# Kernel optimization log

Measured on AMD Instinct MI355X. Metric: run time of the kernel, lower is better.

Reference implementation:

```python
import jax, jax.numpy as jnp
import numpy as np

# Dims: B samples, D=2048 backbone feature dim (resnet50 fc.in_features),
B, D, G, R, K, C = 16384, 2048, 8, 6, 3, 16


def setup_inputs() -> dict:
    key = jax.random.key(0)
    k0, k1, k2, k3 = jax.random.split(key, 4)
    feats = jax.random.normal(k0, (B, D), dtype=jnp.float32)          # backbone output (dropout=eval identity)
    roi_ids = jax.random.randint(k1, (B,), 0, G)                       # per-sample routing id (roi_names)
    W_reg = jax.random.normal(k2, (G, R, D), dtype=jnp.float32) * 0.02  # reg_heads[roi].weight
    b_reg = jnp.zeros((G, R), dtype=jnp.float32)                       # reg_heads[roi].bias
    W_cls = jax.random.normal(k3, (G, K, C, D), dtype=jnp.float32) * 0.02  # cls_heads[roi][k].weight
    b_cls = jnp.zeros((G, K, C), dtype=jnp.float32)                    # cls_heads[roi][k].bias
    return {"feats": feats, "roi_ids": roi_ids, "W_reg": W_reg, "b_reg": b_reg,
            "W_cls": W_cls, "b_cls": b_cls}


def reference(feats, roi_ids, W_reg, b_reg, W_cls, b_cls):
    # Original loop applies, per sample i, the Linear heads of roi_names[i].
    # Vectorized: compute all-ROI head outputs densely, then gather the routed one.
    # (Same math per sample; dropout is identity in eval mode.)
    reg_all = jnp.einsum('bd,grd->bgr', feats, W_reg) + b_reg[None]        # [B, G, R]
    cls_all = jnp.einsum('bd,gkcd->bgkc', feats, W_cls) + b_cls[None]      # [B, G, K, C]
    reg = jnp.take_along_axis(reg_all, roi_ids[:, None, None], axis=1)[:, 0]            # [B, R]
    cls = jnp.take_along_axis(cls_all, roi_ids[:, None, None, None], axis=1)[:, 0]      # [B, K, C]
    return reg, cls
```

## Files before the change

### kernel.cpp

```cpp
#include <hip/hip_runtime.h>
#include <hip/hip_bf16.h>

#define NB   16384
#define ND   2048
#define NG   8
#define NR   6
#define NKC  48
#define NOUT 54
#define KW   512
#define NT16 (NB / 16 + NG)
#define LROW 136
#define BM   32
#define KC   128
#define NCH  (ND / KC)
#define MAXT (NB / BM + NG)

typedef __attribute__((ext_vector_type(8))) short short8_t;
typedef __attribute__((ext_vector_type(4))) float f32x4;

__device__ __forceinline__ unsigned short f2bf(float x) {
    union { float f; unsigned u; } v; v.f = x;
    unsigned r = v.u + 0x7FFFu + ((v.u >> 16) & 1u);
    return (unsigned short)(r >> 16);
}

__device__ __forceinline__ short8_t cvt8(float4 a, float4 b) {
    short8_t s;
    s[0] = (short)f2bf(a.x); s[1] = (short)f2bf(a.y);
    s[2] = (short)f2bf(a.z); s[3] = (short)f2bf(a.w);
    s[4] = (short)f2bf(b.x); s[5] = (short)f2bf(b.y);
    s[6] = (short)f2bf(b.z); s[7] = (short)f2bf(b.w);
    return s;
}

__device__ __forceinline__ short8_t as_s8(float4 v) {
    union { float4 f; short8_t s; } u; u.f = v; return u.s;
}

#define WAITV(N) do { asm volatile("s_waitcnt vmcnt(" #N ")" ::: "memory"); \
                      __builtin_amdgcn_sched_barrier(0); } while (0)

__global__ void hist_kernel(const int* __restrict__ roi, int* __restrict__ counts) {
    int i = blockIdx.x * 256 + threadIdx.x;
    int g = roi[i];
    int lane = threadIdx.x & 63;
    #pragma unroll
    for (int gg = 0; gg < NG; ++gg) {
        unsigned long long m = __ballot(g == gg);
        if (m && lane == (int)(__ffsll((unsigned long long)m) - 1))
            atomicAdd(&counts[gg], (int)__popcll(m));
    }
}

__global__ void scatter_kernel(const int* __restrict__ roi, const int* __restrict__ counts,
                               int* __restrict__ ranks, int* __restrict__ perm) {
    int off[NG];
    int acc = 0;
    #pragma unroll
    for (int gg = 0; gg < NG; ++gg) { off[gg] = acc; acc += counts[gg]; }
    int i = blockIdx.x * 256 + threadIdx.x;
    int g = roi[i];
    int lane = threadIdx.x & 63;
    #pragma unroll
    for (int gg = 0; gg < NG; ++gg) {
        unsigned long long m = __ballot(g == gg);
        if (!m) continue;
        int leader = (int)(__ffsll((unsigned long long)m) - 1);
        int base = 0;
        if (lane == leader) base = atomicAdd(&ranks[gg], (int)__popcll(m));
        base = __shfl(base, leader);
        if (g == gg) {
            int rank = (int)__popcll(m & ((1ull << lane) - 1ull));
            perm[off[gg] + base + rank] = i;
        }
    }
}

__global__ void scatter1_kernel(const int* __restrict__ roi, int* __restrict__ cnt,
                                int* __restrict__ perm) {
    int i = blockIdx.x * 256 + threadIdx.x;
    int g = roi[i];
    int lane = threadIdx.x & 63;
    #pragma unroll
    for (int gg = 0; gg < NG; ++gg) {
        unsigned long long m = __ballot(g == gg);
        if (!m) continue;
        int leader = (int)(__ffsll((unsigned long long)m) - 1);
        int base = 0;
        if (lane == leader) base = atomicAdd(&cnt[gg], (int)__popcll(m));
        base = __shfl(base, leader);
        if (g == gg) {
            int rank = (int)__popcll(m & ((1ull << lane) - 1ull));
            perm[gg * NB + base + rank] = i;
        }
    }
}

__global__ void wconv_kernel(const float* __restrict__ Wreg, const float* __restrict__ Wcls,
                             short* __restrict__ Wbf) {
    int u = blockIdx.x * 256 + threadIdx.x;
    int l = u & 63;
    int q = (u >> 6) & 7;
    int c = (u >> 9) & 31;
    int g = u >> 14;
    int n = q >> 1, ks = q & 1;
    int row = n * 16 + (l & 15);
    int k   = c * 64 + ks * 32 + (l >> 4) * 8;
    short8_t v = {0, 0, 0, 0, 0, 0, 0, 0};
    if (row < NOUT) {
        const float* s = (row < NR) ? Wreg + (size_t)(g * NR + row) * ND + k
                                    : Wcls + (size_t)(g * NKC + row - NR) * ND + k;
        float4 a = *(const float4*)s;
        float4 b = *(const float4*)(s + 4);
        v = cvt8(a, b);
    }
    *(short8_t*)(Wbf + (size_t)u * 8) = v;
}

__launch_bounds__(256, 3)
__global__ void gemm_asm_kernel(const float* __restrict__ feats,
                                const short* __restrict__ Wbf,
                                const float* __restrict__ breg, const float* __restrict__ bcls,
                                const int* __restrict__ counts, const int* __restrict__ perm,
                                float* __restrict__ out, int stride) {
    __shared__ float sacc[3][16][66];

    int tid = threadIdx.x, w = tid >> 6, l = tid & 63, lr = l & 15, lq = l >> 4;
    int t = blockIdx.x;

    int ts[NG + 1]; ts[0] = 0;
    int off[NG]; int acc_ = 0;
    #pragma unroll
    for (int gg = 0; gg < NG; ++gg) {
        int c = counts[gg];
        off[gg] = stride ? gg * stride : acc_;
        acc_ += c;
        ts[gg + 1] = ts[gg] + (c + 15) / 16;
    }
    if (t >= ts[NG]) return;
    int g = 0;
    #pragma unroll
    for (int gg = 0; gg < NG; ++gg) if (t >= ts[gg + 1]) g = gg + 1;
    int gcnt  = counts[g];
    int goff  = off[g];
    int rbase = (t - ts[g]) * 16;
    int nvalid = gcnt - rbase; if (nvalid > 16) nvalid = 16;

    int r = rbase + lr; if (r >= gcnt) r = gcnt - 1;
    int smp = perm[goff + r];
    const char* aB = (const char*)(feats + (size_t)smp * ND + w * KW + lq * 8);
    const char* bB = (const char*)(Wbf + (size_t)g * 131072 + (size_t)w * 8 * 4096 + l * 8);

    f32x4 acc0 = {0,0,0,0}, acc1 = {0,0,0,0}, acc2 = {0,0,0,0}, acc3 = {0,0,0,0};
    float4 xa0, xa1, xa2, xa3, ya0, ya1, ya2, ya3;
    float4 xb0, xb1, xb2, xb3, xb4, xb5, xb6, xb7;
    float4 yb0, yb1, yb2, yb3, yb4, yb5, yb6, yb7;

#define ISSUE(cc, P) do {                                                               \
        const char* a_ = aB + (cc) * 256;                                               \
        asm volatile("global_load_dwordx4 %0, %1, off"            : "=v"(P##a0) : "v"(a_) : "memory"); \
        asm volatile("global_load_dwordx4 %0, %1, off offset:16"  : "=v"(P##a1) : "v"(a_) : "memory"); \
        asm volatile("global_load_dwordx4 %0, %1, off offset:128" : "=v"(P##a2) : "v"(a_) : "memory"); \
        asm volatile("global_load_dwordx4 %0, %1, off offset:144" : "=v"(P##a3) : "v"(a_) : "memory"); \
        const char* b_  = bB + (cc) * 8192;                                             \
        const char* b2_ = b_ + 4096;                                                    \
        asm volatile("global_load_dwordx4 %0, %1, off"             : "=v"(P##b0) : "v"(b_)  : "memory"); \
        asm volatile("global_load_dwordx4 %0, %1, off offset:1024" : "=v"(P##b1) : "v"(b_)  : "memory"); \
        asm volatile("global_load_dwordx4 %0, %1, off offset:2048" : "=v"(P##b2) : "v"(b_)  : "memory"); \
        asm volatile("global_load_dwordx4 %0, %1, off offset:3072" : "=v"(P##b3) : "v"(b_)  : "memory"); \
        asm volatile("global_load_dwordx4 %0, %1, off"             : "=v"(P##b4) : "v"(b2_) : "memory"); \
        asm volatile("global_load_dwordx4 %0, %1, off offset:1024" : "=v"(P##b5) : "v"(b2_) : "memory"); \
        asm volatile("global_load_dwordx4 %0, %1, off offset:2048" : "=v"(P##b6) : "v"(b2_) : "memory"); \
        asm volatile("global_load_dwordx4 %0, %1, off offset:3072" : "=v"(P##b7) : "v"(b2_) : "memory"); \
    } while (0)

#define CMP(P) do {                                                                     \
        short8_t af0 = cvt8(P##a0, P##a1), af1 = cvt8(P##a2, P##a3);                    \
        acc0 = __builtin_amdgcn_mfma_f32_16x16x32_bf16(af0, as_s8(P##b0), acc0, 0, 0, 0); \
        acc1 = __builtin_amdgcn_mfma_f32_16x16x32_bf16(af0, as_s8(P##b2), acc1, 0, 0, 0); \
        acc2 = __builtin_amdgcn_mfma_f32_16x16x32_bf16(af0, as_s8(P##b4), acc2, 0, 0, 0); \
        acc3 = __builtin_amdgcn_mfma_f32_16x16x32_bf16(af0, as_s8(P##b6), acc3, 0, 0, 0); \
        acc0 = __builtin_amdgcn_mfma_f32_16x16x32_bf16(af1, as_s8(P##b1), acc0, 0, 0, 0); \
        acc1 = __builtin_amdgcn_mfma_f32_16x16x32_bf16(af1, as_s8(P##b3), acc1, 0, 0, 0); \
        acc2 = __builtin_amdgcn_mfma_f32_16x16x32_bf16(af1, as_s8(P##b5), acc2, 0, 0, 0); \
        acc3 = __builtin_amdgcn_mfma_f32_16x16x32_bf16(af1, as_s8(P##b7), acc3, 0, 0, 0); \
    } while (0)

    ISSUE(0, x); ISSUE(1, y);
    WAITV(12); CMP(x); ISSUE(2, x);
    WAITV(12); CMP(y); ISSUE(3, y);
    WAITV(12); CMP(x); ISSUE(4, x);
    WAITV(12); CMP(y); ISSUE(5, y);
    WAITV(12); CMP(x); ISSUE(6, x);
    WAITV(12); CMP(y); ISSUE(7, y);
    WAITV(12); CMP(x);
    WAITV(0);  CMP(y);
#undef ISSUE
#undef CMP

    if (w > 0) {
        #pragma unroll
        for (int n = 0; n < 4; ++n) {
            f32x4 v = (n == 0) ? acc0 : (n == 1) ? acc1 : (n == 2) ? acc2 : acc3;
            #pragma unroll
            for (int j = 0; j < 4; ++j)
                sacc[w - 1][lq * 4 + j][n * 16 + lr] = v[j];
        }
    }
    __syncthreads();

    if (w == 0) {
        const int B6 = NB * NR;
        #pragma unroll
        for (int n = 0; n < 4; ++n) {
            f32x4 a = (n == 0) ? acc0 : (n == 1) ? acc1 : (n == 2) ? acc2 : acc3;
            int col = n * 16 + lr;
            if (col < NOUT) {
                #pragma unroll
                for (int j = 0; j < 4; ++j) {
                    int row = lq * 4 + j;
                    if (row < nvalid) {
                        float v = a[j] + sacc[0][row][col] + sacc[1][row][col] + sacc[2][row][col];
                        int s2 = perm[goff + rbase + row];
                        if (col < NR) out[s2 * NR + col] = v + breg[g * NR + col];
                        else          out[B6 + s2 * NKC + (col - NR)] = v + bcls[g * NKC + (col - NR)];
                    }
                }
            }
        }
    }
}

__launch_bounds__(256, 3)
__global__ void gemm_kernel(const float* __restrict__ feats,
                            const float* __restrict__ Wreg, const float* __restrict__ breg,
                            const float* __restrict__ Wcls, const float* __restrict__ bcls,
                            const int* __restrict__ counts, const int* __restrict__ perm,
                            float* __restrict__ out, int stride) {
    __shared__ __align__(16) short Bsh[2][64][LROW];
    __shared__ int sRow[BM];

    int ts[NG + 1]; ts[0] = 0;
    int off[NG]; int acc = 0;
    #pragma unroll
    for (int gg = 0; gg < NG; ++gg) {
        int c = counts[gg];
        off[gg] = stride ? gg * stride : acc;
        acc += c;
        ts[gg + 1] = ts[gg] + (c + BM - 1) / BM;
    }
    int b = blockIdx.x;
    if (b >= ts[NG]) return;
    int g = 0;
    #pragma unroll
    for (int gg = 0; gg < NG; ++gg) if (b >= ts[gg + 1]) g = gg + 1;
    int gcnt  = counts[g];
    int goff  = off[g];
    int rbase = (b - ts[g]) * BM;
    int nvalid = gcnt - rbase; if (nvalid > BM) nvalid = BM;

    int tid = threadIdx.x;
    if (tid < BM) {
        int r = rbase + tid;
        if (r >= gcnt) r = gcnt - 1;
        sRow[tid] = perm[goff + r];
    }
    __syncthreads();

    int rB = tid >> 2;
    int cq = tid & 3;
    const float* wsrc = nullptr;
    if (rB < NR)        wsrc = Wreg + ((size_t)g * NR + rB) * ND + cq * 32;
    else if (rB < NOUT) wsrc = Wcls + ((size_t)g * NKC + (rB - NR)) * ND + cq * 32;

    int w = tid >> 6, l = tid & 63, lr = l & 15, lq = l >> 4;
    int mt = w & 1, nh = w >> 1;
    const float* aptr = feats + (size_t)sRow[mt * 16 + lr] * ND + lq * 8;
    const short* brp = (const short*)&Bsh[0][0][0] + (nh * 32 + lr) * LROW + lq * 8;

    f32x4 acc0 = {0, 0, 0, 0}, acc1 = {0, 0, 0, 0};
    float4 rb[8];

    if (wsrc) {
        #pragma unroll
        for (int i = 0; i < 8; ++i) rb[i] = *(const float4*)(wsrc + 4 * i);
    } else {
        #pragma unroll
        for (int i = 0; i < 8; ++i) rb[i] = make_float4(0.f, 0.f, 0.f, 0.f);
    }
    {
        short* bw = &Bsh[0][rB][cq * 32];
        #pragma unroll
        for (int j = 0; j < 4; ++j) *(short8_t*)(bw + 8 * j) = cvt8(rb[2 * j], rb[2 * j + 1]);
    }
    __syncthreads();

    #pragma unroll
    for (int c = 0; c < NCH; ++c) {
        const int cur = c & 1, nxt = cur ^ 1;
        if (c + 1 < NCH && wsrc) {
            const float* s = wsrc + (c + 1) * KC;
            #pragma unroll
            for (int i = 0; i < 8; ++i) rb[i] = *(const float4*)(s + 4 * i);
        }
        const short* bp = brp + cur * (64 * LROW);
        const float* ap = aptr + c * KC;
        #pragma unroll
        for (int ks = 0; ks < 4; ++ks) {
            float4 a0 = *(const float4*)(ap + ks * 32);
            float4 a1 = *(const float4*)(ap + ks * 32 + 4);
            short8_t af = cvt8(a0, a1);
            short8_t b0 = *(const short8_t*)(bp + ks * 32);
            short8_t b1 = *(const short8_t*)(bp + 16 * LROW + ks * 32);
            acc0 = __builtin_amdgcn_mfma_f32_16x16x32_bf16(af, b0, acc0, 0, 0, 0);
            acc1 = __builtin_amdgcn_mfma_f32_16x16x32_bf16(af, b1, acc1, 0, 0, 0);
        }
        if (c + 1 < NCH && wsrc) {
            short* bw = &Bsh[nxt][rB][cq * 32];
            #pragma unroll
            for (int j = 0; j < 4; ++j) *(short8_t*)(bw + 8 * j) = cvt8(rb[2 * j], rb[2 * j + 1]);
        } else if (c + 1 < NCH) {
            short8_t z = {0,0,0,0,0,0,0,0};
            short* bw = &Bsh[nxt][rB][cq * 32];
            #pragma unroll
            for (int j = 0; j < 4; ++j) *(short8_t*)(bw + 8 * j) = z;
        }
        __syncthreads();
    }

    const int B6 = NB * NR;
    #pragma unroll
    for (int n = 0; n < 2; ++n) {
        f32x4 v = n ? acc1 : acc0;
        int col = nh * 32 + n * 16 + lr;
        if (col < NOUT) {
            #pragma unroll
            for (int j = 0; j < 4; ++j) {
                int row = mt * 16 + lq * 4 + j;
                if (row < nvalid) {
                    int smp = sRow[row];
                    if (col < NR) out[smp * NR + col] = v[j] + breg[g * NR + col];
                    else          out[B6 + smp * NKC + (col - NR)] = v[j] + bcls[g * NKC + (col - NR)];
                }
            }
        }
    }
}

__global__ void fallback_kernel(const float* __restrict__ feats, const int* __restrict__ roi,
                                const float* __restrict__ Wreg, const float* __restrict__ breg,
                                const float* __restrict__ Wcls, const float* __restrict__ bcls,
                                float* __restrict__ out) {
    int i = blockIdx.x;
    int lane = threadIdx.x;
    int g = roi[i];
    const float* frow = feats + (size_t)i * ND;
    float f[32];
    #pragma unroll
    for (int q = 0; q < 32; ++q) f[q] = frow[lane + 64 * q];
    for (int o = 0; o < NOUT; ++o) {
        const float* wrow = (o < NR) ? Wreg + ((size_t)g * NR + o) * ND
                                     : Wcls + ((size_t)g * NKC + (o - NR)) * ND;
        float p = 0.f;
        #pragma unroll
        for (int q = 0; q < 32; ++q) p += f[q] * wrow[lane + 64 * q];
        #pragma unroll
        for (int s = 32; s; s >>= 1) p += __shfl_xor(p, s);
        if (lane == 0) {
            if (o < NR) out[i * NR + o] = p + breg[g * NR + o];
            else        out[NB * NR + i * NKC + (o - NR)] = p + bcls[g * NKC + (o - NR)];
        }
    }
}

extern "C" void kernel_launch(void* const* d_in, const int* in_sizes, int n_in,
                              void* d_out, int out_size, void* d_ws, size_t ws_size,
                              hipStream_t stream) {
    const float* feats = (const float*)d_in[0];
    const int*   roi   = (const int*)d_in[1];
    const float* Wreg  = (const float*)d_in[2];
    const float* breg  = (const float*)d_in[3];
    const float* Wcls  = (const float*)d_in[4];
    const float* bcls  = (const float*)d_in[5];
    float* out = (float*)d_out;

    const size_t wbfBytes = (size_t)NG * 131072 * 2;
    const size_t need_t1 = wbfBytes + 256 + (size_t)NG * NB * 4;
    const size_t need_t3 = 256 + (size_t)NB * 4;

    if (ws_size >= need_t1) {
        short* Wbf = (short*)d_ws;
        int* cnt  = (int*)((char*)d_ws + wbfBytes);
        int* perm = cnt + 64;
        hipMemsetAsync(cnt, 0, 8 * sizeof(int), stream);
        wconv_kernel<<<512, 256, 0, stream>>>(Wreg, Wcls, Wbf);
        scatter1_kernel<<<NB / 256, 256, 0, stream>>>(roi, cnt, perm);
        gemm_asm_kernel<<<NT16, 256, 0, stream>>>(feats, Wbf, breg, bcls, cnt, perm, out, NB);
    } else if (ws_size >= need_t3) {
        int* counts = (int*)d_ws;
        int* ranks  = counts + 8;
        int* perm   = counts + 64;
        hipMemsetAsync(counts, 0, 16 * sizeof(int), stream);
        hist_kernel<<<NB / 256, 256, 0, stream>>>(roi, counts);
        scatter_kernel<<<NB / 256, 256, 0, stream>>>(roi, counts, ranks, perm);
        gemm_kernel<<<MAXT, 256, 0, stream>>>(feats, Wreg, breg, Wcls, bcls, counts, perm, out, 0);
    } else {
        fallback_kernel<<<NB, 64, 0, stream>>>(feats, roi, Wreg, breg, Wcls, bcls, out);
    }
}
```

Baseline: 72.19 us.

## Fuse prep kernels and widen GEMM row tile to 32 samples

Merges the ROI scatter and the weight bf16 conversion into one prep kernel, removing a launch. The routed GEMM now handles 32 rows per block instead of 16, so each weight fragment loaded from global memory feeds twice as many MFMAs, halving total weight traffic. Row indices are staged in shared memory and the bias load is hoisted out of the inner loop. The cost is more registers per thread (occupancy hint lowered to 2 blocks per CU), fewer blocks in the grid, and more padding waste on each group's last tile.

```diff
diff --git a/kernel.cpp b/kernel.cpp
--- a/kernel.cpp
+++ b/kernel.cpp
@@ -2,13 +2,12 @@
 #include <hip/hip_bf16.h>
 
 #define NB   16384
+#define NG   8
 #define ND   2048
-#define NG   8
 #define NR   6
 #define NKC  48
 #define NOUT 54
-#define KW   512
-#define NT16 (NB / 16 + NG)
+#define NT32 (NB / 32 + NG)
 #define LROW 136
 #define BM   32
 #define KC   128
@@ -76,92 +75,100 @@
     }
 }
 
-__global__ void scatter1_kernel(const int* __restrict__ roi, int* __restrict__ cnt,
-                                int* __restrict__ perm) {
-    int i = blockIdx.x * 256 + threadIdx.x;
-    int g = roi[i];
-    int lane = threadIdx.x & 63;
-    #pragma unroll
-    for (int gg = 0; gg < NG; ++gg) {
-        unsigned long long m = __ballot(g == gg);
-        if (!m) continue;
-        int leader = (int)(__ffsll((unsigned long long)m) - 1);
-        int base = 0;
-        if (lane == leader) base = atomicAdd(&cnt[gg], (int)__popcll(m));
-        base = __shfl(base, leader);
-        if (g == gg) {
-            int rank = (int)__popcll(m & ((1ull << lane) - 1ull));
-            perm[gg * NB + base + rank] = i;
-        }
-    }
-}
-
-__global__ void wconv_kernel(const float* __restrict__ Wreg, const float* __restrict__ Wcls,
-                             short* __restrict__ Wbf) {
-    int u = blockIdx.x * 256 + threadIdx.x;
-    int l = u & 63;
-    int q = (u >> 6) & 7;
-    int c = (u >> 9) & 31;
-    int g = u >> 14;
-    int n = q >> 1, ks = q & 1;
-    int row = n * 16 + (l & 15);
-    int k   = c * 64 + ks * 32 + (l >> 4) * 8;
-    short8_t v = {0, 0, 0, 0, 0, 0, 0, 0};
-    if (row < NOUT) {
-        const float* s = (row < NR) ? Wreg + (size_t)(g * NR + row) * ND + k
-                                    : Wcls + (size_t)(g * NKC + row - NR) * ND + k;
-        float4 a = *(const float4*)s;
-        float4 b = *(const float4*)(s + 4);
-        v = cvt8(a, b);
-    }
-    *(short8_t*)(Wbf + (size_t)u * 8) = v;
-}
-
-__launch_bounds__(256, 3)
-__global__ void gemm_asm_kernel(const float* __restrict__ feats,
-                                const short* __restrict__ Wbf,
-                                const float* __restrict__ breg, const float* __restrict__ bcls,
-                                const int* __restrict__ counts, const int* __restrict__ perm,
-                                float* __restrict__ out, int stride) {
-    __shared__ float sacc[3][16][66];
-
-    int tid = threadIdx.x, w = tid >> 6, l = tid & 63, lr = l & 15, lq = l >> 4;
+__global__ void prep_kernel(const int* __restrict__ roi, int* __restrict__ cnt,
+                            int* __restrict__ perm,
+                            const float* __restrict__ Wreg, const float* __restrict__ Wcls,
+                            short* __restrict__ Wbf) {
+    if (blockIdx.x < 64) {
+        int i = blockIdx.x * 256 + threadIdx.x;
+        int g = roi[i];
+        int lane = threadIdx.x & 63;
+        #pragma unroll
+        for (int gg = 0; gg < NG; ++gg) {
+            unsigned long long m = __ballot(g == gg);
+            if (!m) continue;
+            int leader = (int)(__ffsll((unsigned long long)m) - 1);
+            int base = 0;
+            if (lane == leader) base = atomicAdd(&cnt[gg], (int)__popcll(m));
+            base = __shfl(base, leader);
+            if (g == gg) {
+                int rank = (int)__popcll(m & ((1ull << lane) - 1ull));
+                perm[gg * NB + base + rank] = i;
+            }
+        }
+    } else {
+        int u = (blockIdx.x - 64) * 256 + threadIdx.x;
+        int l = u & 63;
+        int q = (u >> 6) & 7;
+        int c = (u >> 9) & 31;
+        int g = u >> 14;
+        int n = q >> 1, ks = q & 1;
+        int row = n * 16 + (l & 15);
+        int k   = c * 64 + ks * 32 + (l >> 4) * 8;
+        short8_t v = {0, 0, 0, 0, 0, 0, 0, 0};
+        if (row < NOUT) {
+            const float* s = (row < NR) ? Wreg + (size_t)(g * NR + row) * ND + k
+                                        : Wcls + (size_t)(g * NKC + row - NR) * ND + k;
+            float4 a = *(const float4*)s;
+            float4 b = *(const float4*)(s + 4);
+            v = cvt8(a, b);
+        }
+        *(short8_t*)(Wbf + (size_t)u * 8) = v;
+    }
+}
+
+__launch_bounds__(256, 2)
+__global__ void gemm32_kernel(const float* __restrict__ feats,
+                              const short* __restrict__ Wbf,
+                              const float* __restrict__ breg, const float* __restrict__ bcls,
+                              const int* __restrict__ counts, const int* __restrict__ perm,
+                              float* __restrict__ out) {
+    __shared__ float sacc[3][32][66];
+    __shared__ int sRow[32];
+
+    int tid = threadIdx.x, kh = tid >> 6, l = tid & 63, lr = l & 15, lq = l >> 4;
     int t = blockIdx.x;
 
     int ts[NG + 1]; ts[0] = 0;
-    int off[NG]; int acc_ = 0;
-    #pragma unroll
-    for (int gg = 0; gg < NG; ++gg) {
-        int c = counts[gg];
-        off[gg] = stride ? gg * stride : acc_;
-        acc_ += c;
-        ts[gg + 1] = ts[gg] + (c + 15) / 16;
-    }
+    #pragma unroll
+    for (int gg = 0; gg < NG; ++gg) ts[gg + 1] = ts[gg] + ((counts[gg] + 31) >> 5);
     if (t >= ts[NG]) return;
     int g = 0;
     #pragma unroll
     for (int gg = 0; gg < NG; ++gg) if (t >= ts[gg + 1]) g = gg + 1;
     int gcnt  = counts[g];
-    int goff  = off[g];
-    int rbase = (t - ts[g]) * 16;
-    int nvalid = gcnt - rbase; if (nvalid > 16) nvalid = 16;
-
-    int r = rbase + lr; if (r >= gcnt) r = gcnt - 1;
-    int smp = perm[goff + r];
-    const char* aB = (const char*)(feats + (size_t)smp * ND + w * KW + lq * 8);
-    const char* bB = (const char*)(Wbf + (size_t)g * 131072 + (size_t)w * 8 * 4096 + l * 8);
+    int rbase = (t - ts[g]) * 32;
+    int nvalid = gcnt - rbase; if (nvalid > 32) nvalid = 32;
+
+    if (tid < 32) {
+        int r = rbase + tid;
+        if (r >= gcnt) r = gcnt - 1;
+        sRow[tid] = perm[g * NB + r];
+    }
+    __syncthreads();
+
+    const char* aB0 = (const char*)(feats + (size_t)sRow[lr] * ND      + kh * 512 + lq * 8);
+    const char* aB1 = (const char*)(feats + (size_t)sRow[16 + lr] * ND + kh * 512 + lq * 8);
+    const char* bB  = (const char*)(Wbf + (size_t)g * 131072 + (size_t)kh * 8 * 4096 + l * 8);
 
     f32x4 acc0 = {0,0,0,0}, acc1 = {0,0,0,0}, acc2 = {0,0,0,0}, acc3 = {0,0,0,0};
-    float4 xa0, xa1, xa2, xa3, ya0, ya1, ya2, ya3;
+    f32x4 acc4 = {0,0,0,0}, acc5 = {0,0,0,0}, acc6 = {0,0,0,0}, acc7 = {0,0,0,0};
+    float4 xa0, xa1, xa2, xa3, xa4, xa5, xa6, xa7;
+    float4 ya0, ya1, ya2, ya3, ya4, ya5, ya6, ya7;
     float4 xb0, xb1, xb2, xb3, xb4, xb5, xb6, xb7;
     float4 yb0, yb1, yb2, yb3, yb4, yb5, yb6, yb7;
 
 #define ISSUE(cc, P) do {                                                               \
-        const char* a_ = aB + (cc) * 256;                                               \
+        const char* a_ = aB0 + (cc) * 256;                                              \
         asm volatile("global_load_dwordx4 %0, %1, off"            : "=v"(P##a0) : "v"(a_) : "memory"); \
         asm volatile("global_load_dwordx4 %0, %1, off offset:16"  : "=v"(P##a1) : "v"(a_) : "memory"); \
         asm volatile("global_load_dwordx4 %0, %1, off offset:128" : "=v"(P##a2) : "v"(a_) : "memory"); \
         asm volatile("global_load_dwordx4 %0, %1, off offset:144" : "=v"(P##a3) : "v"(a_) : "memory"); \
+        const char* a2_ = aB1 + (cc) * 256;                                             \
+        asm volatile("global_load_dwordx4 %0, %1, off"            : "=v"(P##a4) : "v"(a2_) : "memory"); \
+        asm volatile("global_load_dwordx4 %0, %1, off offset:16"  : "=v"(P##a5) : "v"(a2_) : "memory"); \
+        asm volatile("global_load_dwordx4 %0, %1, off offset:128" : "=v"(P##a6) : "v"(a2_) : "memory"); \
+        asm volatile("global_load_dwordx4 %0, %1, off offset:144" : "=v"(P##a7) : "v"(a2_) : "memory"); \
         const char* b_  = bB + (cc) * 8192;                                             \
         const char* b2_ = b_ + 4096;                                                    \
         asm volatile("global_load_dwordx4 %0, %1, off"             : "=v"(P##b0) : "v"(b_)  : "memory"); \
@@ -175,55 +182,76 @@
     } while (0)
 
 #define CMP(P) do {                                                                     \
-        short8_t af0 = cvt8(P##a0, P##a1), af1 = cvt8(P##a2, P##a3);                    \
-        acc0 = __builtin_amdgcn_mfma_f32_16x16x32_bf16(af0, as_s8(P##b0), acc0, 0, 0, 0); \
-        acc1 = __builtin_amdgcn_mfma_f32_16x16x32_bf16(af0, as_s8(P##b2), acc1, 0, 0, 0); \
-        acc2 = __builtin_amdgcn_mfma_f32_16x16x32_bf16(af0, as_s8(P##b4), acc2, 0, 0, 0); \
-        acc3 = __builtin_amdgcn_mfma_f32_16x16x32_bf16(af0, as_s8(P##b6), acc3, 0, 0, 0); \
-        acc0 = __builtin_amdgcn_mfma_f32_16x16x32_bf16(af1, as_s8(P##b1), acc0, 0, 0, 0); \
-        acc1 = __builtin_amdgcn_mfma_f32_16x16x32_bf16(af1, as_s8(P##b3), acc1, 0, 0, 0); \
-        acc2 = __builtin_amdgcn_mfma_f32_16x16x32_bf16(af1, as_s8(P##b5), acc2, 0, 0, 0); \
-        acc3 = __builtin_amdgcn_mfma_f32_16x16x32_bf16(af1, as_s8(P##b7), acc3, 0, 0, 0); \
+        short8_t af00 = cvt8(P##a0, P##a1), af01 = cvt8(P##a2, P##a3);                  \
+        short8_t af10 = cvt8(P##a4, P##a5), af11 = cvt8(P##a6, P##a7);                  \
+        acc0 = __builtin_amdgcn_mfma_f32_16x16x32_bf16(af00, as_s8(P##b0), acc0, 0, 0, 0); \
+        acc1 = __builtin_amdgcn_mfma_f32_16x16x32_bf16(af00, as_s8(P##b2), acc1, 0, 0, 0); \
+        acc2 = __builtin_amdgcn_mfma_f32_16x16x32_bf16(af00, as_s8(P##b4), acc2, 0, 0, 0); \
+        acc3 = __builtin_amdgcn_mfma_f32_16x16x32_bf16(af00, as_s8(P##b6), acc3, 0, 0, 0); \
+        acc4 = __builtin_amdgcn_mfma_f32_16x16x32_bf16(af10, as_s8(P##b0), acc4, 0, 0, 0); \
+        acc5 = __builtin_amdgcn_mfma_f32_16x16x32_bf16(af10, as_s8(P##b2), acc5, 0, 0, 0); \
+        acc6 = __builtin_amdgcn_mfma_f32_16x16x32_bf16(af10, as_s8(P##b4), acc6, 0, 0, 0); \
+        acc7 = __builtin_amdgcn_mfma_f32_16x16x32_bf16(af10, as_s8(P##b6), acc7, 0, 0, 0); \
+        acc0 = __builtin_amdgcn_mfma_f32_16x16x32_bf16(af01, as_s8(P##b1), acc0, 0, 0, 0); \
+        acc1 = __builtin_amdgcn_mfma_f32_16x16x32_bf16(af01, as_s8(P##b3), acc1, 0, 0, 0); \
+        acc2 = __builtin_amdgcn_mfma_f32_16x16x32_bf16(af01, as_s8(P##b5), acc2, 0, 0, 0); \
+        acc3 = __builtin_amdgcn_mfma_f32_16x16x32_bf16(af01, as_s8(P##b7), acc3, 0, 0, 0); \
+        acc4 = __builtin_amdgcn_mfma_f32_16x16x32_bf16(af11, as_s8(P##b1), acc4, 0, 0, 0); \
+        acc5 = __builtin_amdgcn_mfma_f32_16x16x32_bf16(af11, as_s8(P##b3), acc5, 0, 0, 0); \
+        acc6 = __builtin_amdgcn_mfma_f32_16x16x32_bf16(af11, as_s8(P##b5), acc6, 0, 0, 0); \
+        acc7 = __builtin_amdgcn_mfma_f32_16x16x32_bf16(af11, as_s8(P##b7), acc7, 0, 0, 0); \
     } while (0)
 
     ISSUE(0, x); ISSUE(1, y);
-    WAITV(12); CMP(x); ISSUE(2, x);
-    WAITV(12); CMP(y); ISSUE(3, y);
-    WAITV(12); CMP(x); ISSUE(4, x);
-    WAITV(12); CMP(y); ISSUE(5, y);
-    WAITV(12); CMP(x); ISSUE(6, x);
-    WAITV(12); CMP(y); ISSUE(7, y);
-    WAITV(12); CMP(x);
+    WAITV(16); CMP(x); ISSUE(2, x);
+    WAITV(16); CMP(y); ISSUE(3, y);
+    WAITV(16); CMP(x); ISSUE(4, x);
+    WAITV(16); CMP(y); ISSUE(5, y);
+    WAITV(16); CMP(x); ISSUE(6, x);
+    WAITV(16); CMP(y); ISSUE(7, y);
+    WAITV(16); CMP(x);
     WAITV(0);  CMP(y);
 #undef ISSUE
 #undef CMP
 
-    if (w > 0) {
-        #pragma unroll
-        for (int n = 0; n < 4; ++n) {
-            f32x4 v = (n == 0) ? acc0 : (n == 1) ? acc1 : (n == 2) ? acc2 : acc3;
-            #pragma unroll
-            for (int j = 0; j < 4; ++j)
-                sacc[w - 1][lq * 4 + j][n * 16 + lr] = v[j];
+    if (kh > 0) {
+        #pragma unroll
+        for (int mt = 0; mt < 2; ++mt) {
+            #pragma unroll
+            for (int n = 0; n < 4; ++n) {
+                f32x4 v = (mt == 0)
+                    ? ((n == 0) ? acc0 : (n == 1) ? acc1 : (n == 2) ? acc2 : acc3)
+                    : ((n == 0) ? acc4 : (n == 1) ? acc5 : (n == 2) ? acc6 : acc7);
+                #pragma unroll
+                for (int j = 0; j < 4; ++j)
+                    sacc[kh - 1][mt * 16 + lq * 4 + j][n * 16 + lr] = v[j];
+            }
         }
     }
     __syncthreads();
 
-    if (w == 0) {
+    if (kh == 0) {
         const int B6 = NB * NR;
         #pragma unroll
-        for (int n = 0; n < 4; ++n) {
-            f32x4 a = (n == 0) ? acc0 : (n == 1) ? acc1 : (n == 2) ? acc2 : acc3;
-            int col = n * 16 + lr;
-            if (col < NOUT) {
-                #pragma unroll
-                for (int j = 0; j < 4; ++j) {
-                    int row = lq * 4 + j;
-                    if (row < nvalid) {
-                        float v = a[j] + sacc[0][row][col] + sacc[1][row][col] + sacc[2][row][col];
-                        int s2 = perm[goff + rbase + row];
-                        if (col < NR) out[s2 * NR + col] = v + breg[g * NR + col];
-                        else          out[B6 + s2 * NKC + (col - NR)] = v + bcls[g * NKC + (col - NR)];
+        for (int mt = 0; mt < 2; ++mt) {
+            #pragma unroll
+            for (int n = 0; n < 4; ++n) {
+                f32x4 a = (mt == 0)
+                    ? ((n == 0) ? acc0 : (n == 1) ? acc1 : (n == 2) ? acc2 : acc3)
+                    : ((n == 0) ? acc4 : (n == 1) ? acc5 : (n == 2) ? acc6 : acc7);
+                int col = n * 16 + lr;
+                if (col < NOUT) {
+                    float bias = (col < NR) ? breg[g * NR + col] : bcls[g * NKC + (col - NR)];
+                    #pragma unroll
+                    for (int j = 0; j < 4; ++j) {
+                        int row = mt * 16 + lq * 4 + j;
+                        if (row < nvalid) {
+                            float v = a[j] + sacc[0][row][col] + sacc[1][row][col]
+                                           + sacc[2][row][col] + bias;
+                            int s2 = sRow[row];
+                            if (col < NR) out[s2 * NR + col] = v;
+                            else          out[B6 + s2 * NKC + (col - NR)] = v;
+                        }
                     }
                 }
             }
@@ -390,12 +418,11 @@
 
     if (ws_size >= need_t1) {
         short* Wbf = (short*)d_ws;
-        int* cnt  = (int*)((char*)d_ws + wbfBytes);
-        int* perm = cnt + 64;
-        hipMemsetAsync(cnt, 0, 8 * sizeof(int), stream);
-        wconv_kernel<<<512, 256, 0, stream>>>(Wreg, Wcls, Wbf);
-        scatter1_kernel<<<NB / 256, 256, 0, stream>>>(roi, cnt, perm);
-        gemm_asm_kernel<<<NT16, 256, 0, stream>>>(feats, Wbf, breg, bcls, cnt, perm, out, NB);
+        int* cnt   = (int*)((char*)d_ws + wbfBytes);
+        int* perm  = cnt + 64;
+        hipMemsetAsync(cnt, 0, 64, stream);
+        prep_kernel<<<576, 256, 0, stream>>>(roi, cnt, perm, Wreg, Wcls, Wbf);
+        gemm32_kernel<<<NT32, 256, 0, stream>>>(feats, Wbf, breg, bcls, cnt, perm, out);
     } else if (ws_size >= need_t3) {
         int* counts = (int*)d_ws;
         int* ranks  = counts + 8;
```

Result: faster. 70.59 us (-2.2%).
